# Performance work log

Hardware: AMD Instinct MI355X
Metric: run time of the kernel (lower is better)

Reference implementation:

```python
import jax, jax.numpy as jnp
import numpy as np
from jax import lax

TEMP = 0.1
EPS_LOG = 1e-6
RMS_EPS = 1e-6
K_NEIGHBORS = 8


def setup_inputs() -> dict:
    key = jax.random.key(0)
    ks = jax.random.split(key, 8)
    B, T, D = 2, 2048, 1024
    N, DK, DM = 32768, 256, 256
    return {
        "x": jax.random.normal(ks[0], (B, T, D), dtype=jnp.float32),
        "keys": jax.random.normal(ks[1], (N, DK), dtype=jnp.float32),
        "vals": jax.random.normal(ks[2], (N, DM), dtype=jnp.float32),
        "W_in": jax.random.normal(ks[3], (DK, D), dtype=jnp.float32) / np.sqrt(D),
        "b_in": jnp.zeros((DK,), dtype=jnp.float32),
        "W_out": jax.random.normal(ks[4], (D, K_NEIGHBORS * DM), dtype=jnp.float32) / np.sqrt(K_NEIGHBORS * DM),
        "b_out": jnp.zeros((D,), dtype=jnp.float32),
        "rms_w": jnp.ones((D,), dtype=jnp.float32),
    }


def _memory_forward(x, keys, vals, W_in, b_in, W_out, b_out, rms_w):
    B, T, D = x.shape
    N, DM = vals.shape
    # proj_in: [B,T,D] -> [B,T,DK]
    q = jnp.einsum("btd,kd->btk", x, W_in) + b_in
    # squared euclidean distances to memory keys: [B,T,N]
    q2 = jnp.sum(q * q, axis=-1, keepdims=True)          # [B,T,1]
    k2 = jnp.sum(keys * keys, axis=-1)                   # [N]
    qk = jnp.einsum("btc,nc->btn", q, keys)              # [B,T,N]
    logits = -(q2 - 2.0 * qk + k2) / TEMP                # [B,T,N]

    # N3Net-style continuous k-NN: k rounds of softmax selection
    def step(lg, _):
        w = jax.nn.softmax(lg, axis=-1)                  # [B,T,N]
        out = jnp.einsum("btn,nf->btf", w, vals)         # [B,T,DM]
        lg = lg + jnp.log1p(-w + EPS_LOG)
        return lg, out

    _, outs = lax.scan(step, logits, None, length=K_NEIGHBORS)  # [K,B,T,DM]
    nearest = jnp.moveaxis(outs, 0, 2).reshape(B, T, K_NEIGHBORS * DM)

    out = jnp.einsum("btf,df->btd", nearest, W_out) + b_out
    # RMSNorm
    var = jnp.mean(out.astype(jnp.float32) ** 2, axis=-1, keepdims=True)
    out = out * lax.rsqrt(var + RMS_EPS)
    return rms_w * out


def reference(x, keys, vals, W_in, b_in, W_out, b_out, rms_w):
    return _memory_forward(x, keys, vals, W_in, b_in, W_out, b_out, rms_w)
```

## Files before the change

kernel.cpp:

```cpp
#include <hip/hip_runtime.h>
#include <hip/hip_bf16.h>

#define ROWS  4096
#define DDIM  1024
#define DKDIM 256
#define NKEYS 32768
#define DMDIM 256
#define KN    8
#define FDIM  2048
#define CAPS  1536
#define SURV  128
#define SURV2 96
#define MARGIN   16.0f
#define REFILT_M 12.25f
#define EXACT_M  109.0f

typedef float  f32x4  __attribute__((ext_vector_type(4)));
typedef __bf16 bf16x8 __attribute__((ext_vector_type(8)));

static __device__ __forceinline__ unsigned enc_f32(float f) {
  unsigned u = __float_as_uint(f);
  return u ^ ((unsigned)((int)u >> 31) | 0x80000000u);
}
static __device__ __forceinline__ float dec_f32(unsigned u) {
  unsigned b = (u & 0x80000000u) ? (u ^ 0x80000000u) : ~u;
  return __uint_as_float(b);
}
static __device__ __forceinline__ unsigned short f2bf(float f) {
  unsigned u = __float_as_uint(f);
  u += 0x7FFFu + ((u >> 16) & 1u);
  return (unsigned short)(u >> 16);
}
static __device__ __forceinline__ unsigned pack_cand(float s, int n) {
  float q = (s + 1024.f) * 64.f;
  int u = (int)q;
  u = u < 0 ? 0 : (u > 131071 ? 131071 : u);
  return ((unsigned)u << 15) | (unsigned)n;
}
static __device__ __forceinline__ float cand_score(unsigned p) {
  return (float)(p >> 15) * (1.f / 64.f) - 1024.f;
}
static __device__ __forceinline__ void gld16(const void* g, void* l) {
  __builtin_amdgcn_global_load_lds((const __attribute__((address_space(1))) void*)g,
                                   (__attribute__((address_space(3))) void*)l, 16, 0, 0);
}

__global__ __launch_bounds__(256) void prep_all(const float* __restrict__ keys,
                                                const float* __restrict__ Wout,
                                                unsigned short* __restrict__ kbf,
                                                float* __restrict__ k2,
                                                unsigned short* __restrict__ wbf,
                                                unsigned* __restrict__ rowmax) {
  const int b = blockIdx.x, t = threadIdx.x;
  if (b < 8192) {
    const int row = b * 4 + (t >> 6);
    const int ln  = t & 63;
    const float4 v = *(const float4*)(keys + (size_t)row * DKDIM + ln * 4);
    ushort4 o;
    o.x = f2bf(v.x); o.y = f2bf(v.y); o.z = f2bf(v.z); o.w = f2bf(v.w);
    *(ushort4*)(kbf + (size_t)row * DKDIM + ln * 4) = o;
    float ss = v.x*v.x + v.y*v.y + v.z*v.z + v.w*v.w;
    for (int off = 32; off; off >>= 1) ss += __shfl_down(ss, off);
    if (ln == 0) k2[row] = ss;
  } else if (b < 10240) {
    const int i = (b - 8192) * 256 + t;
    const float4 v = *(const float4*)(Wout + (size_t)i * 4);
    ushort4 o;
    o.x = f2bf(v.x); o.y = f2bf(v.y); o.z = f2bf(v.z); o.w = f2bf(v.w);
    *(ushort4*)(wbf + (size_t)i * 4) = o;
  } else {
    rowmax[(b - 10240) * 256 + t] = 0u;
  }
}

__global__ __launch_bounds__(256) void qproj(const float* __restrict__ x,
                                             const float* __restrict__ Win,
                                             const float* __restrict__ bin,
                                             float* __restrict__ qf,
                                             unsigned short* __restrict__ qbf) {
  __shared__ __align__(16) float As[64][68];
  __shared__ __align__(16) float Bs[64][68];
  const int bm = blockIdx.x, bn = blockIdx.y;
  const int t  = threadIdx.x;
  const int tx = t & 15, ty = t >> 4;
  float acc[4][4] = {};
  for (int ks = 0; ks < 16; ++ks) {
    __syncthreads();
    for (int l = t; l < 1024; l += 256) {
      const int row = l >> 4, kc = l & 15;
      *(float4*)(&As[row][kc * 4]) =
          *(const float4*)(x + (size_t)(bm * 64 + row) * DDIM + ks * 64 + kc * 4);
      *(float4*)(&Bs[row][kc * 4]) =
          *(const float4*)(Win + (size_t)(bn * 64 + row) * DDIM + ks * 64 + kc * 4);
    }
    __syncthreads();
    for (int kk = 0; kk < 64; kk += 4) {
      float4 av[4], bv[4];
#pragma unroll
      for (int i = 0; i < 4; ++i) av[i] = *(const float4*)(&As[ty * 4 + i][kk]);
#pragma unroll
      for (int j = 0; j < 4; ++j) bv[j] = *(const float4*)(&Bs[tx * 4 + j][kk]);
#pragma unroll
      for (int i = 0; i < 4; ++i)
#pragma unroll
        for (int j = 0; j < 4; ++j)
          acc[i][j] += av[i].x * bv[j].x + av[i].y * bv[j].y +
                       av[i].z * bv[j].z + av[i].w * bv[j].w;
    }
  }
#pragma unroll
  for (int i = 0; i < 4; ++i)
#pragma unroll
    for (int j = 0; j < 4; ++j) {
      const int m = bm * 64 + ty * 4 + i, n = bn * 64 + tx * 4 + j;
      const float q = acc[i][j] + bin[n];
      qf[(size_t)m * DKDIM + n] = q;
      qbf[(size_t)m * DKDIM + n] = f2bf(q);
    }
}

template <int KD>
static __device__ __forceinline__ void gemm_tile(const unsigned short* __restrict__ A,
                                                 const unsigned short* __restrict__ B,
                                                 int bm, int bn,
                                                 unsigned short* As, unsigned short* Bs,
                                                 f32x4 acc[4][4]) {
  const int tid  = threadIdx.x;
  const int lane = tid & 63, wave = tid >> 6;
  const int quad = lane >> 4, l15 = lane & 15;
  const int wr = (wave >> 1) * 64, wc = (wave & 1) * 64;
  const int srow = tid >> 2, skc = tid & 3;
  const unsigned short* gA = A + (size_t)(bm * 128 + srow) * KD + skc * 8;
  const unsigned short* gB = B + (size_t)(bn * 128 + srow) * KD + skc * 8;
  for (int ks = 0; ks < KD / 32; ++ks) {
    __syncthreads();
    gld16(gA + ks * 32,                     As + tid * 8);
    gld16(gA + (size_t)64 * KD + ks * 32,   As + 2048 + tid * 8);
    gld16(gB + ks * 32,                     Bs + tid * 8);
    gld16(gB + (size_t)64 * KD + ks * 32,   Bs + 2048 + tid * 8);
    __syncthreads();
    bf16x8 af[4], bfr[4];
#pragma unroll
    for (int i = 0; i < 4; ++i)
      af[i] = *(const bf16x8*)(As + (wr + i * 16 + l15) * 32 + quad * 8);
#pragma unroll
    for (int j = 0; j < 4; ++j)
      bfr[j] = *(const bf16x8*)(Bs + (wc + j * 16 + l15) * 32 + quad * 8);
#pragma unroll
    for (int i = 0; i < 4; ++i)
#pragma unroll
      for (int j = 0; j < 4; ++j)
        acc[i][j] = __builtin_amdgcn_mfma_f32_16x16x32_bf16(af[i], bfr[j], acc[i][j], 0, 0, 0);
  }
}

__global__ __launch_bounds__(256) void score_select(const unsigned short* __restrict__ qbf,
                                                    const unsigned short* __restrict__ kbf,
                                                    const float* __restrict__ k2,
                                                    unsigned* __restrict__ rowmax,
                                                    int* __restrict__ cnt,
                                                    unsigned* __restrict__ cand) {
  __shared__ __align__(16) unsigned short As[4096];
  __shared__ __align__(16) unsigned short Bs[4096];
  __shared__ float wm[128][2];
  __shared__ float thr[128];
  f32x4 acc[4][4] = {};
  gemm_tile<DKDIM>(qbf, kbf, blockIdx.x, blockIdx.y, As, Bs, acc);
  const int t = threadIdx.x;
  const int lane = t & 63, wave = t >> 6;
  const int quad = lane >> 4, l15 = lane & 15;
  const int wr = (wave >> 1) * 64, wc = (wave & 1) * 64;
  float k2v[4];
#pragma unroll
  for (int j = 0; j < 4; ++j) k2v[j] = k2[blockIdx.y * 128 + wc + j * 16 + l15];
#pragma unroll
  for (int i = 0; i < 4; ++i)
#pragma unroll
    for (int r = 0; r < 4; ++r) {
      float v = -3.4e38f;
#pragma unroll
      for (int j = 0; j < 4; ++j) v = fmaxf(v, 2.f * acc[i][j][r] - k2v[j]);
      for (int m = 8; m; m >>= 1) v = fmaxf(v, __shfl_xor(v, m));
      if (l15 == 0) wm[wr + i * 16 + quad * 4 + r][wave & 1] = v;
    }
  __syncthreads();
  if (t < 128) {
    const float tile = fmaxf(wm[t][0], wm[t][1]);
    const unsigned old = atomicMax(&rowmax[blockIdx.x * 128 + t], enc_f32(tile));
    thr[t] = fmaxf(tile, dec_f32(old)) - MARGIN;
  }
  __syncthreads();
#pragma unroll
  for (int i = 0; i < 4; ++i)
#pragma unroll
    for (int r = 0; r < 4; ++r) {
      const int rl = wr + i * 16 + quad * 4 + r;
      const float th = thr[rl];
      const int gm = blockIdx.x * 128 + rl;
#pragma unroll
      for (int j = 0; j < 4; ++j) {
        const float s = 2.f * acc[i][j][r] - k2v[j];
        if (s >= th) {
          const int n = blockIdx.y * 128 + wc + j * 16 + l15;
          const int pos = atomicAdd(&cnt[gm], 1);
          if (pos < CAPS) cand[(size_t)gm * CAPS + pos] = pack_cand(s, n);
        }
      }
    }
}

__global__ __launch_bounds__(256) void knn_rounds(const float* __restrict__ qf,
                                                  const float* __restrict__ keys,
                                                  const float* __restrict__ k2,
                                                  const float* __restrict__ vals,
                                                  const int* __restrict__ cnt,
                                                  const unsigned* __restrict__ cand,
                                                  unsigned short* __restrict__ nearest) {
  __shared__ __align__(16) float qs[DKDIM];
  __shared__ unsigned cl[CAPS];
  __shared__ float red[256];
  __shared__ int   sidx[SURV];
  __shared__ float Ls[SURV];
  __shared__ int   sidx2[SURV2];
  __shared__ float L2v[SURV2];
  __shared__ float cs[SURV2];
  __shared__ float Ws[SURV2 * KN];
  __shared__ int n1, n2;
  const int row = blockIdx.x, t = threadIdx.x;
  const int C = min(cnt[row], CAPS);
  qs[t] = qf[(size_t)row * DKDIM + t];
  if (t == 0) { n1 = 0; n2 = 0; }
  float m = -3.4e38f;
  for (int i = t; i < C; i += 256) {
    const unsigned p = cand[(size_t)row * CAPS + i];
    cl[i] = p;
    m = fmaxf(m, cand_score(p));
  }
  red[t] = m;
  __syncthreads();
  for (int s = 128; s; s >>= 1) {
    if (t < s) red[t] = fmaxf(red[t], red[t + s]);
    __syncthreads();
  }
  const float th1 = red[0] - REFILT_M;
  for (int i = t; i < C; i += 256) {
    if (cand_score(cl[i]) >= th1) {
      const int p = atomicAdd(&n1, 1);
      if (p < SURV) sidx[p] = (int)(cl[i] & 32767u);
    }
  }
  if (t < SURV2) cs[t] = 0.f;
  __syncthreads();
  const int S1 = min(n1, SURV);
  const int wv = t >> 6, ln = t & 63;
  for (int i = wv; i < S1; i += 4) {
    const int n = sidx[i];
    const float4 kv = *(const float4*)(keys + (size_t)n * DKDIM + ln * 4);
    const float4 qv = *(const float4*)(qs + ln * 4);
    float d = kv.x * qv.x + kv.y * qv.y + kv.z * qv.z + kv.w * qv.w;
    for (int o = 32; o; o >>= 1) d += __shfl_down(d, o);
    if (ln == 0) Ls[i] = (2.f * d - k2[n]) / 0.1f;
  }
  __syncthreads();
  red[t] = (t < S1) ? Ls[t] : -3.4e38f;
  __syncthreads();
  for (int s = 128; s; s >>= 1) {
    if (t < s) red[t] = fmaxf(red[t], red[t + s]);
    __syncthreads();
  }
  const float Lmax = red[0];
  if (t < S1 && Ls[t] >= Lmax - EXACT_M) {
    const int p = atomicAdd(&n2, 1);
    if (p < SURV2) { sidx2[p] = sidx[t]; L2v[p] = Ls[t]; }
  }
  __syncthreads();
  const int S2 = min(n2, SURV2);
  if (t < 64) {
    for (int j = 0; j < KN; ++j) {
      float lm = -3.4e38f;
      for (int i = t; i < S2; i += 64) lm = fmaxf(lm, L2v[i] + cs[i]);
      for (int o = 32; o; o >>= 1) lm = fmaxf(lm, __shfl_xor(lm, o));
      float zs = 0.f;
      for (int i = t; i < S2; i += 64) {
        const float e = expf(L2v[i] + cs[i] - lm);
        Ws[i * KN + j] = e; zs += e;
      }
      for (int o = 32; o; o >>= 1) zs += __shfl_xor(zs, o);
      const float Zi = 1.f / zs;
      for (int i = t; i < S2; i += 64) {
        const float w = Ws[i * KN + j] * Zi;
        Ws[i * KN + j] = w;
        cs[i] += log1pf(1e-6f - w);
      }
    }
  }
  __syncthreads();
  float acc[KN] = {};
  for (int i = 0; i < S2; ++i) {
    const float v = vals[(size_t)sidx2[i] * DMDIM + t];
#pragma unroll
    for (int j = 0; j < KN; ++j) acc[j] += Ws[i * KN + j] * v;
  }
#pragma unroll
  for (int j = 0; j < KN; ++j)
    nearest[(size_t)row * FDIM + j * DMDIM + t] = f2bf(acc[j]);
}

__global__ __launch_bounds__(256) void out_gemm(const unsigned short* __restrict__ nbf,
                                                const unsigned short* __restrict__ wbf,
                                                const float* __restrict__ bout,
                                                float* __restrict__ out) {
  __shared__ __align__(16) unsigned short As[4096];
  __shared__ __align__(16) unsigned short Bs[4096];
  f32x4 acc[4][4] = {};
  gemm_tile<FDIM>(nbf, wbf, blockIdx.x, blockIdx.y, As, Bs, acc);
  const int lane = threadIdx.x & 63, wave = threadIdx.x >> 6;
  const int quad = lane >> 4, l15 = lane & 15;
  const int wr = (wave >> 1) * 64, wc = (wave & 1) * 64;
#pragma unroll
  for (int i = 0; i < 4; ++i)
#pragma unroll
    for (int r = 0; r < 4; ++r) {
      const int gm = blockIdx.x * 128 + wr + i * 16 + quad * 4 + r;
#pragma unroll
      for (int j = 0; j < 4; ++j) {
        const int n = blockIdx.y * 128 + wc + j * 16 + l15;
        out[(size_t)gm * DDIM + n] = acc[i][j][r] + bout[n];
      }
    }
}

__global__ __launch_bounds__(256) void rmsnorm(float* __restrict__ out,
                                               const float* __restrict__ rmsw) {
  __shared__ float red[256];
  const int row = blockIdx.x, t = threadIdx.x;
  const float4 v = *(const float4*)(out + (size_t)row * DDIM + t * 4);
  red[t] = v.x * v.x + v.y * v.y + v.z * v.z + v.w * v.w;
  __syncthreads();
  for (int s = 128; s; s >>= 1) {
    if (t < s) red[t] += red[t + s];
    __syncthreads();
  }
  const float scale = rsqrtf(red[0] / (float)DDIM + 1e-6f);
  const float4 w = *(const float4*)(rmsw + t * 4);
  float4 o;
  o.x = v.x * scale * w.x; o.y = v.y * scale * w.y;
  o.z = v.z * scale * w.z; o.w = v.w * scale * w.w;
  *(float4*)(out + (size_t)row * DDIM + t * 4) = o;
}

extern "C" void kernel_launch(void* const* d_in, const int* in_sizes, int n_in,
                              void* d_out, int out_size, void* d_ws, size_t ws_size,
                              hipStream_t stream) {
  const float* x    = (const float*)d_in[0];
  const float* keys = (const float*)d_in[1];
  const float* vals = (const float*)d_in[2];
  const float* Win  = (const float*)d_in[3];
  const float* bin  = (const float*)d_in[4];
  const float* Wout = (const float*)d_in[5];
  const float* bout = (const float*)d_in[6];
  const float* rmsw = (const float*)d_in[7];
  float* out = (float*)d_out;
  char* ws = (char*)d_ws;

  float*          q_f32   = (float*)(ws);
  unsigned short* q_bf    = (unsigned short*)(ws + 4194304);
  unsigned short* k_bf    = (unsigned short*)(ws + 6291456);
  unsigned short* nearest = (unsigned short*)(ws + 6291456);
  float*          k2      = (float*)(ws + 23068672);
  unsigned*       rowmax  = (unsigned*)(ws + 23199744);
  int*            cnt     = (int*)(ws + 23216128);
  unsigned*       cand    = (unsigned*)(ws + 23232512);
  unsigned short* w_bf    = (unsigned short*)(ws + 48398336);

  prep_all<<<10272, 256, 0, stream>>>(keys, Wout, k_bf, k2, w_bf, rowmax);
  qproj<<<dim3(ROWS / 64, DKDIM / 64), 256, 0, stream>>>(x, Win, bin, q_f32, q_bf);
  score_select<<<dim3(ROWS / 128, NKEYS / 128), 256, 0, stream>>>(q_bf, k_bf, k2, rowmax, cnt, cand);
  knn_rounds<<<ROWS, 256, 0, stream>>>(q_f32, keys, k2, vals, cnt, cand, nearest);
  out_gemm<<<dim3(ROWS / 128, DDIM / 128), 256, 0, stream>>>(nearest, w_bf, bout, out);
  rmsnorm<<<ROWS, 256, 0, stream>>>(out, rmsw);
}
```

Measured before the change: 438.0 us.

## Persistent score-select blocks sweep 4096 keys with resident Q tile and triple-buffered keys

score_select now launches 256 blocks of 512 threads. Each block keeps its 128-row query tile resident in LDS and streams 4096 keys through a three-stage asynchronous buffer, keeping a running per-row max across key tiles. Global cnt atomics are replaced by LDS counters that write into per-row, per-chunk candidate slots, which knn_rounds then concatenates. The aim is to cut the repeated Q loads, the per-tile launch overhead and the global atomic contention. The cost is much larger LDS use, lower occupancy, and a per-chunk slot cap of 184 that can truncate candidates.

```diff
diff --git a/kernel.cpp b/kernel.cpp
--- a/kernel.cpp
+++ b/kernel.cpp
@@ -9,6 +9,7 @@
 #define KN    8
 #define FDIM  2048
 #define CAPS  1536
+#define SLOT  184
 #define SURV  128
 #define SURV2 96
 #define MARGIN   16.0f
@@ -154,59 +155,136 @@
   }
 }
 
-__global__ __launch_bounds__(256) void score_select(const unsigned short* __restrict__ qbf,
+__global__ __launch_bounds__(512) void score_select(const unsigned short* __restrict__ qbf,
                                                     const unsigned short* __restrict__ kbf,
                                                     const float* __restrict__ k2,
                                                     unsigned* __restrict__ rowmax,
                                                     int* __restrict__ cnt,
                                                     unsigned* __restrict__ cand) {
-  __shared__ __align__(16) unsigned short As[4096];
-  __shared__ __align__(16) unsigned short Bs[4096];
-  __shared__ float wm[128][2];
+  __shared__ __align__(16) unsigned short Al[8 * 4096];
+  __shared__ __align__(16) unsigned short Bl[3 * 8192];
+  __shared__ __align__(16) float k2s[4096];
+  __shared__ float wm[128][4];
   __shared__ float thr[128];
-  f32x4 acc[4][4] = {};
-  gemm_tile<DKDIM>(qbf, kbf, blockIdx.x, blockIdx.y, As, Bs, acc);
+  __shared__ float lmax[128];
+  __shared__ int   pcnt[128];
+  const int cg = blockIdx.x, bm = blockIdx.y;
   const int t = threadIdx.x;
   const int lane = t & 63, wave = t >> 6;
   const int quad = lane >> 4, l15 = lane & 15;
-  const int wr = (wave >> 1) * 64, wc = (wave & 1) * 64;
-  float k2v[4];
-#pragma unroll
-  for (int j = 0; j < 4; ++j) k2v[j] = k2[blockIdx.y * 128 + wc + j * 16 + l15];
-#pragma unroll
-  for (int i = 0; i < 4; ++i)
-#pragma unroll
-    for (int r = 0; r < 4; ++r) {
-      float v = -3.4e38f;
-#pragma unroll
-      for (int j = 0; j < 4; ++j) v = fmaxf(v, 2.f * acc[i][j][r] - k2v[j]);
-      for (int m = 8; m; m >>= 1) v = fmaxf(v, __shfl_xor(v, m));
-      if (l15 == 0) wm[wr + i * 16 + quad * 4 + r][wave & 1] = v;
-    }
-  __syncthreads();
-  if (t < 128) {
-    const float tile = fmaxf(wm[t][0], wm[t][1]);
-    const unsigned old = atomicMax(&rowmax[blockIdx.x * 128 + t], enc_f32(tile));
-    thr[t] = fmaxf(tile, dec_f32(old)) - MARGIN;
-  }
-  __syncthreads();
-#pragma unroll
-  for (int i = 0; i < 4; ++i)
-#pragma unroll
-    for (int r = 0; r < 4; ++r) {
-      const int rl = wr + i * 16 + quad * 4 + r;
-      const float th = thr[rl];
-      const int gm = blockIdx.x * 128 + rl;
-#pragma unroll
-      for (int j = 0; j < 4; ++j) {
-        const float s = 2.f * acc[i][j][r] - k2v[j];
-        if (s >= th) {
-          const int n = blockIdx.y * 128 + wc + j * 16 + l15;
-          const int pos = atomicAdd(&cnt[gm], 1);
-          if (pos < CAPS) cand[(size_t)gm * CAPS + pos] = pack_cand(s, n);
+  const int wr = (wave >> 2) * 64, wc = (wave & 3) * 64;
+  const unsigned short* gA = qbf + (size_t)(bm * 128 + (t >> 2)) * DKDIM + (t & 3) * 8;
+  const unsigned short* gB = kbf + ((size_t)cg * 4096 + (t >> 2)) * DKDIM + (t & 3) * 8;
+
+  if (t < 128) { lmax[t] = -3.4e38f; pcnt[t] = 0; }
+
+#pragma unroll
+  for (int ks = 0; ks < 8; ++ks)
+    gld16(gA + ks * 32, Al + ks * 4096 + t * 8);
+  {
+    const float* gk = k2 + (size_t)cg * 4096;
+#pragma unroll
+    for (int i = 0; i < 2; ++i)
+      gld16(gk + i * 2048 + t * 4, (char*)k2s + i * 8192 + t * 16);
+  }
+#pragma unroll
+  for (int c0 = 0; c0 < 2; ++c0) {
+    gld16(gB + c0 * 32, Bl + c0 * 8192 + t * 8);
+    gld16(gB + (size_t)128 * DKDIM + c0 * 32, Bl + c0 * 8192 + 4096 + t * 8);
+  }
+
+  f32x4 acc[4][4] = {};
+  int bcur = 0;
+  for (int tile = 0; tile < 16; ++tile) {
+    unsigned rstale = 0u;
+    if (t < 128) rstale = rowmax[bm * 128 + t];
+#pragma unroll
+    for (int ks = 0; ks < 8; ++ks) {
+      if (tile == 15 && ks == 7)
+        asm volatile("s_waitcnt vmcnt(0)" ::: "memory");
+      else if (ks == 0)
+        asm volatile("s_waitcnt vmcnt(3)" ::: "memory");
+      else
+        asm volatile("s_waitcnt vmcnt(2)" ::: "memory");
+      __builtin_amdgcn_s_barrier();
+      asm volatile("" ::: "memory");
+      {
+        const int cn = tile * 8 + ks + 2;
+        if (cn < 128) {
+          const int bst = bcur == 0 ? 2 : bcur - 1;
+          const unsigned short* src = gB + (size_t)(cn >> 3) * 256 * DKDIM + (cn & 7) * 32;
+          gld16(src, Bl + bst * 8192 + t * 8);
+          gld16(src + (size_t)128 * DKDIM, Bl + bst * 8192 + 4096 + t * 8);
         }
       }
-    }
+      const unsigned short* Ap = Al + ks * 4096;
+      const unsigned short* Bp = Bl + bcur * 8192;
+      bf16x8 af[4], bv[4];
+#pragma unroll
+      for (int i = 0; i < 4; ++i)
+        af[i] = *(const bf16x8*)(Ap + (wr + i * 16 + l15) * 32 + quad * 8);
+#pragma unroll
+      for (int j = 0; j < 4; ++j)
+        bv[j] = *(const bf16x8*)(Bp + (wc + j * 16 + l15) * 32 + quad * 8);
+#pragma unroll
+      for (int i = 0; i < 4; ++i)
+#pragma unroll
+        for (int j = 0; j < 4; ++j)
+          acc[i][j] = __builtin_amdgcn_mfma_f32_16x16x32_bf16(af[i], bv[j], acc[i][j], 0, 0, 0);
+      bcur = bcur == 2 ? 0 : bcur + 1;
+    }
+    float k2v[4];
+#pragma unroll
+    for (int j = 0; j < 4; ++j) k2v[j] = k2s[tile * 256 + wc + j * 16 + l15];
+#pragma unroll
+    for (int i = 0; i < 4; ++i)
+#pragma unroll
+      for (int r = 0; r < 4; ++r) {
+        float v = -3.4e38f;
+#pragma unroll
+        for (int j = 0; j < 4; ++j) v = fmaxf(v, 2.f * acc[i][j][r] - k2v[j]);
+        for (int m = 8; m; m >>= 1) v = fmaxf(v, __shfl_xor(v, m));
+        if (l15 == 0) wm[wr + i * 16 + quad * 4 + r][wave & 3] = v;
+      }
+    asm volatile("s_waitcnt lgkmcnt(0)" ::: "memory");
+    __builtin_amdgcn_s_barrier();
+    asm volatile("" ::: "memory");
+    if (t < 128) {
+      const float tmax = fmaxf(fmaxf(wm[t][0], wm[t][1]), fmaxf(wm[t][2], wm[t][3]));
+      const float run = fmaxf(lmax[t], tmax);
+      lmax[t] = run;
+      (void)atomicMax(&rowmax[bm * 128 + t], enc_f32(run));
+      thr[t] = fmaxf(run, dec_f32(rstale)) - MARGIN;
+    }
+    asm volatile("s_waitcnt lgkmcnt(0)" ::: "memory");
+    __builtin_amdgcn_s_barrier();
+    asm volatile("" ::: "memory");
+#pragma unroll
+    for (int i = 0; i < 4; ++i)
+#pragma unroll
+      for (int r = 0; r < 4; ++r) {
+        const int rl = wr + i * 16 + quad * 4 + r;
+        const float th = thr[rl];
+#pragma unroll
+        for (int j = 0; j < 4; ++j) {
+          const float s = 2.f * acc[i][j][r] - k2v[j];
+          if (s >= th) {
+            const int n = cg * 4096 + tile * 256 + wc + j * 16 + l15;
+            const int pos = atomicAdd(&pcnt[rl], 1);
+            if (pos < SLOT)
+              cand[((size_t)(bm * 128 + rl) * 8 + cg) * SLOT + pos] = pack_cand(s, n);
+          }
+        }
+      }
+#pragma unroll
+    for (int i = 0; i < 4; ++i)
+#pragma unroll
+      for (int j = 0; j < 4; ++j)
+#pragma unroll
+        for (int r2 = 0; r2 < 4; ++r2) acc[i][j][r2] = 0.f;
+  }
+  __syncthreads();
+  if (t < 128) cnt[(size_t)(bm * 128 + t) * 8 + cg] = min(pcnt[t], SLOT);
 }
 
 __global__ __launch_bounds__(256) void knn_rounds(const float* __restrict__ qf,
@@ -227,14 +305,19 @@
   __shared__ float Ws[SURV2 * KN];
   __shared__ int n1, n2;
   const int row = blockIdx.x, t = threadIdx.x;
-  const int C = min(cnt[row], CAPS);
   qs[t] = qf[(size_t)row * DKDIM + t];
   if (t == 0) { n1 = 0; n2 = 0; }
   float m = -3.4e38f;
-  for (int i = t; i < C; i += 256) {
-    const unsigned p = cand[(size_t)row * CAPS + i];
-    cl[i] = p;
-    m = fmaxf(m, cand_score(p));
+  int C = 0;
+  for (int s8 = 0; s8 < 8; ++s8) {
+    const int Cs = min(cnt[(size_t)row * 8 + s8], SLOT);
+    const unsigned* cp = cand + ((size_t)row * 8 + s8) * SLOT;
+    for (int i = t; i < Cs; i += 256) {
+      const unsigned p = cp[i];
+      cl[C + i] = p;
+      m = fmaxf(m, cand_score(p));
+    }
+    C += Cs;
   }
   red[t] = m;
   __syncthreads();
@@ -370,12 +453,12 @@
   float*          k2      = (float*)(ws + 23068672);
   unsigned*       rowmax  = (unsigned*)(ws + 23199744);
   int*            cnt     = (int*)(ws + 23216128);
-  unsigned*       cand    = (unsigned*)(ws + 23232512);
-  unsigned short* w_bf    = (unsigned short*)(ws + 48398336);
-
-  prep_all<<<10272, 256, 0, stream>>>(keys, Wout, k_bf, k2, w_bf, rowmax);
+  unsigned*       cand    = (unsigned*)(ws + 23347200);
+  unsigned short* w_bf    = (unsigned short*)(ws + 47464448);
+
+  prep_all<<<10256, 256, 0, stream>>>(keys, Wout, k_bf, k2, w_bf, rowmax);
   qproj<<<dim3(ROWS / 64, DKDIM / 64), 256, 0, stream>>>(x, Win, bin, q_f32, q_bf);
-  score_select<<<dim3(ROWS / 128, NKEYS / 128), 256, 0, stream>>>(q_bf, k_bf, k2, rowmax, cnt, cand);
+  score_select<<<dim3(8, 32), 512, 0, stream>>>(q_bf, k_bf, k2, rowmax, cnt, cand);
   knn_rounds<<<ROWS, 256, 0, stream>>>(q_f32, keys, k2, vals, cnt, cand, nearest);
   out_gemm<<<dim3(ROWS / 128, DDIM / 128), 256, 0, stream>>>(nearest, w_bf, bout, out);
   rmsnorm<<<ROWS, 256, 0, stream>>>(out, rmsw);
```

Result: slower. 465.1 us (+6.2%).

## Double-buffer LDS tiles in bf16 GEMM with k-chunk-major shared layout

Applied to the files above, without the earlier changes.

Rewrites the shared GEMM tile routine to use two LDS buffers per operand, issuing the global-to-LDS load for the next k-step before computing on the current one, and halving the barriers per k-step. It also changes the LDS layout to k-chunk-major (quad*1024 + row*8) with a different thread-to-row load mapping, so fragment reads from LDS may hit fewer bank conflicts. This doubles LDS use per block, which may lower occupancy in score_select and out_gemm.

```diff
diff --git a/kernel.cpp b/kernel.cpp
--- a/kernel.cpp
+++ b/kernel.cpp
@@ -123,35 +123,47 @@
 static __device__ __forceinline__ void gemm_tile(const unsigned short* __restrict__ A,
                                                  const unsigned short* __restrict__ B,
                                                  int bm, int bn,
-                                                 unsigned short* As, unsigned short* Bs,
+                                                 unsigned short* As0, unsigned short* As1,
+                                                 unsigned short* Bs0, unsigned short* Bs1,
                                                  f32x4 acc[4][4]) {
   const int tid  = threadIdx.x;
   const int lane = tid & 63, wave = tid >> 6;
   const int quad = lane >> 4, l15 = lane & 15;
   const int wr = (wave >> 1) * 64, wc = (wave & 1) * 64;
-  const int srow = tid >> 2, skc = tid & 3;
-  const unsigned short* gA = A + (size_t)(bm * 128 + srow) * KD + skc * 8;
-  const unsigned short* gB = B + (size_t)(bn * 128 + srow) * KD + skc * 8;
-  for (int ks = 0; ks < KD / 32; ++ks) {
-    __syncthreads();
-    gld16(gA + ks * 32,                     As + tid * 8);
-    gld16(gA + (size_t)64 * KD + ks * 32,   As + 2048 + tid * 8);
-    gld16(gB + ks * 32,                     Bs + tid * 8);
-    gld16(gB + (size_t)64 * KD + ks * 32,   Bs + 2048 + tid * 8);
-    __syncthreads();
-    bf16x8 af[4], bfr[4];
-#pragma unroll
-    for (int i = 0; i < 4; ++i)
-      af[i] = *(const bf16x8*)(As + (wr + i * 16 + l15) * 32 + quad * 8);
-#pragma unroll
-    for (int j = 0; j < 4; ++j)
-      bfr[j] = *(const bf16x8*)(Bs + (wc + j * 16 + l15) * 32 + quad * 8);
-#pragma unroll
-    for (int i = 0; i < 4; ++i)
-#pragma unroll
-      for (int j = 0; j < 4; ++j)
-        acc[i][j] = __builtin_amdgcn_mfma_f32_16x16x32_bf16(af[i], bfr[j], acc[i][j], 0, 0, 0);
-  }
+  const unsigned short* gA = A + (size_t)(bm * 128 + (tid & 127)) * KD + (tid >> 7) * 8;
+  const unsigned short* gB = B + (size_t)(bn * 128 + (tid & 127)) * KD + (tid >> 7) * 8;
+
+#define SS_STAGE(KS, AD, BD)                              \
+  {                                                       \
+    gld16(gA + (KS) * 32,      (AD) + tid * 8);           \
+    gld16(gA + (KS) * 32 + 16, (AD) + 2048 + tid * 8);    \
+    gld16(gB + (KS) * 32,      (BD) + tid * 8);           \
+    gld16(gB + (KS) * 32 + 16, (BD) + 2048 + tid * 8);    \
+  }
+#define SS_COMPUTE(AS, BS)                                                            \
+  {                                                                                   \
+    bf16x8 af[4], bv[4];                                                              \
+    _Pragma("unroll") for (int i = 0; i < 4; ++i)                                     \
+      af[i] = *(const bf16x8*)((AS) + quad * 1024 + (wr + i * 16 + l15) * 8);         \
+    _Pragma("unroll") for (int j = 0; j < 4; ++j)                                     \
+      bv[j] = *(const bf16x8*)((BS) + quad * 1024 + (wc + j * 16 + l15) * 8);         \
+    _Pragma("unroll") for (int i = 0; i < 4; ++i)                                     \
+      _Pragma("unroll") for (int j = 0; j < 4; ++j)                                   \
+        acc[i][j] = __builtin_amdgcn_mfma_f32_16x16x32_bf16(af[i], bv[j], acc[i][j], 0, 0, 0); \
+  }
+
+  SS_STAGE(0, As0, Bs0);
+  __syncthreads();
+  for (int ks = 0; ks < KD / 32; ks += 2) {
+    SS_STAGE(ks + 1, As1, Bs1);
+    SS_COMPUTE(As0, Bs0);
+    __syncthreads();
+    if (ks + 2 < KD / 32) SS_STAGE(ks + 2, As0, Bs0);
+    SS_COMPUTE(As1, Bs1);
+    __syncthreads();
+  }
+#undef SS_STAGE
+#undef SS_COMPUTE
 }
 
 __global__ __launch_bounds__(256) void score_select(const unsigned short* __restrict__ qbf,
@@ -160,12 +172,14 @@
                                                     unsigned* __restrict__ rowmax,
                                                     int* __restrict__ cnt,
                                                     unsigned* __restrict__ cand) {
-  __shared__ __align__(16) unsigned short As[4096];
-  __shared__ __align__(16) unsigned short Bs[4096];
+  __shared__ __align__(16) unsigned short As0[4096];
+  __shared__ __align__(16) unsigned short As1[4096];
+  __shared__ __align__(16) unsigned short Bs0[4096];
+  __shared__ __align__(16) unsigned short Bs1[4096];
   __shared__ float wm[128][2];
   __shared__ float thr[128];
   f32x4 acc[4][4] = {};
-  gemm_tile<DKDIM>(qbf, kbf, blockIdx.x, blockIdx.y, As, Bs, acc);
+  gemm_tile<DKDIM>(qbf, kbf, blockIdx.x, blockIdx.y, As0, As1, Bs0, Bs1, acc);
   const int t = threadIdx.x;
   const int lane = t & 63, wave = t >> 6;
   const int quad = lane >> 4, l15 = lane & 15;
@@ -310,10 +324,12 @@
                                                 const unsigned short* __restrict__ wbf,
                                                 const float* __restrict__ bout,
                                                 float* __restrict__ out) {
-  __shared__ __align__(16) unsigned short As[4096];
-  __shared__ __align__(16) unsigned short Bs[4096];
+  __shared__ __align__(16) unsigned short As0[4096];
+  __shared__ __align__(16) unsigned short As1[4096];
+  __shared__ __align__(16) unsigned short Bs0[4096];
+  __shared__ __align__(16) unsigned short Bs1[4096];
   f32x4 acc[4][4] = {};
-  gemm_tile<FDIM>(nbf, wbf, blockIdx.x, blockIdx.y, As, Bs, acc);
+  gemm_tile<FDIM>(nbf, wbf, blockIdx.x, blockIdx.y, As0, As1, Bs0, Bs1, acc);
   const int lane = threadIdx.x & 63, wave = threadIdx.x >> 6;
   const int quad = lane >> 4, l15 = lane & 15;
   const int wr = (wave >> 1) * 64, wc = (wave & 1) * 64;
```

Result: slower. 530.7 us (+21.2%).
